# Optimization experiments

Measured on AMD Instinct MI355X. Metric: run time of the kernel, lower is better.

Reference implementation:

```python
import jax, jax.numpy as jnp
import numpy as np

MASK_FILL = -987654321.0


def rotate_every_two(x):
    # pairs (x0, x1) -> (-x1, x0), interleaved back along last dim
    x1 = x[..., 0::2]
    x2 = x[..., 1::2]
    return jnp.stack((-x2, x1), axis=-1).reshape(x.shape)


def setup_inputs() -> dict:
    key = jax.random.key(0)
    ks = jax.random.split(key, 6)
    b, n, dim = 64, 197, 768
    heads, dim_head = 12, 64
    inner = heads * dim_head
    x = jax.random.normal(ks[0], (b, n, dim), dtype=jnp.float32)
    pos_emb = jax.random.normal(ks[1], (1, n, dim_head), dtype=jnp.float32)
    w_qkv = jax.random.normal(ks[2], (dim, 3 * inner), dtype=jnp.float32) * (dim ** -0.5)
    scale = jnp.full((heads,), dim_head ** -0.5, dtype=jnp.float32)
    w_out = jax.random.normal(ks[3], (inner, dim), dtype=jnp.float32) * (inner ** -0.5)
    b_out = jnp.zeros((dim,), dtype=jnp.float32)
    return {"x": x, "pos_emb": pos_emb, "w_qkv": w_qkv, "scale": scale,
            "w_out": w_out, "b_out": b_out}


def reference(x, pos_emb, w_qkv, scale, w_out, b_out):
    b, n, dim = x.shape
    h = scale.shape[0]
    qkv = x @ w_qkv                         # [b, n, 3*inner]
    q, k, v = jnp.split(qkv, 3, axis=-1)
    dh = q.shape[-1] // h
    to_heads = lambda t: t.reshape(b, n, h, dh).transpose(0, 2, 1, 3)  # bhnd
    q, k, v = to_heads(q), to_heads(k), to_heads(v)

    # RoPE: pos_emb [1, n, (2 * dh/2)] -> sin/cos [n, dh/2] -> interleave to [n, dh]
    sc = pos_emb[0].reshape(n, 2, dh // 2)
    sin = jnp.repeat(sc[:, 0], 2, axis=-1)  # [n, dh]
    cos = jnp.repeat(sc[:, 1], 2, axis=-1)
    q = q * cos + rotate_every_two(q) * sin
    k = k * cos + rotate_every_two(k) * sin

    # per-head learnable scale
    dots = jnp.einsum('bhid,bhjd->bhij', q, k) * scale[None, :, None, None]
    # diagonal (LSA) mask
    eye = jnp.eye(n, dtype=bool)
    dots = jnp.where(eye, MASK_FILL, dots)

    attn = jax.nn.softmax(dots, axis=-1)
    out = jnp.einsum('bhij,bhjd->bhid', attn, v)
    out = out.transpose(0, 2, 1, 3).reshape(b, n, h * dh)
    return out @ w_out + b_out
```

## Files before the change

kernel.cpp:

```cpp
#include <hip/hip_runtime.h>
#include <math.h>

#define MASK_FILL_F (-987654321.0f)

typedef unsigned short u16;
typedef unsigned int   u32;

constexpr int Bb   = 64;
constexpr int Ntok = 197;
constexpr int Dim  = 768;
constexpr int Heads= 12;
constexpr int Dh   = 64;
constexpr int Nq3  = 2304;
constexpr int Rows = 12608;
constexpr int Mpad = 12672;

using f32x4  = __attribute__((ext_vector_type(4))) float;
using bf16x8 = __attribute__((ext_vector_type(8))) short;

__device__ __forceinline__ u16 f2bf(float f) {
  u32 u = __float_as_uint(f);
  u = (u + 0x7fffu + ((u >> 16) & 1u)) >> 16;
  return (u16)u;
}

__device__ __forceinline__ void stage16(const void* gp, void* lp) {
  __builtin_amdgcn_global_load_lds(
      (const __attribute__((address_space(1))) u32*)gp,
      (__attribute__((address_space(3))) u32*)lp, 16, 0, 0);
}

__device__ __forceinline__ int sigma6(int M) {
  return (M & 0x23) | (((M >> 3) & 1) << 4) | (((M >> 2) & 1) << 3) |
         (((M >> 4) & 1) << 2);
}

__global__ __launch_bounds__(256) void cvt_bf16(const float* __restrict__ in,
                                                u16* __restrict__ out, int n4) {
  const int i = blockIdx.x * 256 + threadIdx.x;
  if (i < n4) {
    const float4 v = *(const float4*)&in[(size_t)i * 4];
    ushort4 u;
    u.x = f2bf(v.x); u.y = f2bf(v.y); u.z = f2bf(v.z); u.w = f2bf(v.w);
    *(ushort4*)&out[(size_t)i * 4] = u;
  }
}

__global__ __launch_bounds__(256) void transpose_cvt(const float* __restrict__ in,
                                                     u16* __restrict__ out,
                                                     int R, int C) {
  __shared__ float t[32][33];
  const int c0 = blockIdx.x * 32, r0 = blockIdx.y * 32;
  const int tx = threadIdx.x & 31, ty = threadIdx.x >> 5;
#pragma unroll
  for (int rr = ty; rr < 32; rr += 8)
    t[rr][tx] = in[(size_t)(r0 + rr) * C + c0 + tx];
  __syncthreads();
#pragma unroll
  for (int cc = ty; cc < 32; cc += 8)
    out[(size_t)(c0 + cc) * R + r0 + tx] = f2bf(t[tx][cc]);
}

__global__ __launch_bounds__(256) void vtrans(const u16* __restrict__ qkvB,
                                              u16* __restrict__ vT) {
  __shared__ u16 t[64 * 72];
  const int jt = blockIdx.x, bh = blockIdx.y;
  const int b = bh / Heads, h = bh % Heads;
  const int j0 = jt * 64;
  const int tid = threadIdx.x;

  for (int idx = tid; idx < 512; idx += 256) {
    const int jr = idx >> 3, c8 = (idx & 7) * 8;
    const int j = j0 + jr;
    uint4 u = make_uint4(0u, 0u, 0u, 0u);
    if (j < Ntok)
      u = *(const uint4*)(qkvB + (size_t)(b * Ntok + j) * Nq3 + 2 * Dim + h * Dh + c8);
    *(uint4*)&t[jr * 72 + c8] = u;
  }
  __syncthreads();
  for (int idx = tid; idx < 512; idx += 256) {
    const int d = idx >> 3, j8 = (idx & 7) * 8;
    ushort4 lo, hi;
    lo.x = t[(j8 + 0) * 72 + d]; lo.y = t[(j8 + 1) * 72 + d];
    lo.z = t[(j8 + 2) * 72 + d]; lo.w = t[(j8 + 3) * 72 + d];
    hi.x = t[(j8 + 4) * 72 + d]; hi.y = t[(j8 + 5) * 72 + d];
    hi.z = t[(j8 + 6) * 72 + d]; hi.w = t[(j8 + 7) * 72 + d];
    u16* dst = vT + ((size_t)bh * 64 + d) * 256 + j0 + j8;
    *(ushort4*)dst       = lo;
    *(ushort4*)(dst + 4) = hi;
  }
}

constexpr int Kc  = 768;
constexpr int NKT = Kc / 64;
#define KTC(x) ((x) < NKT ? (x) : (NKT - 1))

#define BARM() asm volatile("s_barrier" ::: "memory")
#define VMW4() asm volatile("s_waitcnt vmcnt(4)" ::: "memory")

#define STGA(chunk, kt, BUF) \
  stage16(Ag + (size_t)(m0 + (chunk) * 8 + srow) * Kc + (kt) * 64 + scol, \
          &As[BUF][(chunk) * 512])
#define STGB(chunk, kt, BUF) \
  stage16(Bg + (size_t)(n0 + (chunk) * 8 + srow) * Kc + (kt) * 64 + scol, \
          &Bs[BUF][(chunk) * 512])

#define RDA(BUF, MH) \
  _Pragma("unroll") for (int m_ = 0; m_ < 4; ++m_) \
  _Pragma("unroll") for (int k_ = 0; k_ < 2; ++k_) \
    af[m_][k_] = *(const bf16x8*)&As[BUF][(wr * 128 + (MH) * 64 + m_ * 16 + tx) * 64 \
                                          + (((k_ * 4 + qd) ^ sx) * 8)];
#define RDB(BUF, NH, BFR) \
  _Pragma("unroll") for (int n_ = 0; n_ < 2; ++n_) \
  _Pragma("unroll") for (int k_ = 0; k_ < 2; ++k_) \
    BFR[n_][k_] = *(const bf16x8*)&Bs[BUF][(wc * 64 + (NH) * 32 + n_ * 16 + tx) * 64 \
                                           + (((k_ * 4 + qd) ^ sx) * 8)];

#define MM(MH, NH, BFR) \
  __builtin_amdgcn_s_setprio(1); \
  _Pragma("unroll") for (int m_ = 0; m_ < 4; ++m_) \
  _Pragma("unroll") for (int n_ = 0; n_ < 2; ++n_) \
  _Pragma("unroll") for (int k_ = 0; k_ < 2; ++k_) \
    acc[(MH) * 4 + m_][(NH) * 2 + n_] = __builtin_amdgcn_mfma_f32_16x16x32_bf16( \
        af[m_][k_], BFR[n_][k_], acc[(MH) * 4 + m_][(NH) * 2 + n_], 0, 0, 0); \
  __builtin_amdgcn_s_setprio(0);

template<int TN>
__global__ __launch_bounds__(512, 2) void gemm8p(
    const u16* __restrict__ Ag, const u16* __restrict__ Bg,
    u16* __restrict__ Cb, int Nn, int nwg,
    const float* __restrict__ pe)
{
  __shared__ u16 As[2][256 * 64];
  __shared__ u16 Bs[2][256 * 64];

  const int tid = threadIdx.x, lane = tid & 63, w = tid >> 6;

  const int orig = blockIdx.x;
  const int q8 = nwg >> 3, r8 = nwg & 7;
  const int xcd = orig & 7, sub = orig >> 3;
  const int wgid = (xcd < r8 ? xcd * (q8 + 1) : r8 * (q8 + 1) + (xcd - r8) * q8) + sub;
  const int tm = wgid / TN, tn = wgid % TN;
  const int m0 = tm * 256, n0 = tn * 256;

  const int wr = w >> 2, wc = w & 3;
  const int tx = lane & 15, qd = lane >> 4, sx = tx & 7;

  const int srow = lane >> 3;
  const int scol = ((lane & 7) ^ srow) * 8;
  const int b0 = (w >> 1) * 8 + (w & 1) * 2;

  STGA(w, 0, 0);        STGA(16 + w, 0, 0);
  STGB(b0 + 4, 0, 0);   STGB(b0 + 5, 0, 0);
  STGA(8 + w, 0, 0);    STGA(24 + w, 0, 0);
  STGB(b0, 0, 0);       STGB(b0 + 1, 0, 0);
  STGA(w, 1, 1);        STGA(16 + w, 1, 1);
  STGB(b0 + 4, 1, 1);   STGB(b0 + 5, 1, 1);
  VMW4();
  BARM();

  f32x4  acc[8][4] = {};
  bf16x8 af[4][2], bf0[2][2], bf1[2][2];

#pragma unroll 1
  for (int i = 0; i < NKT / 2; ++i) {
    const int u = 2 * i;
    RDA(0, 0); RDB(0, 0, bf0);
    STGA(8 + w, u + 1, 1); STGA(24 + w, u + 1, 1);
    BARM(); MM(0, 0, bf0); BARM();
    RDB(0, 1, bf1);
    STGB(b0, u + 1, 1); STGB(b0 + 1, u + 1, 1);
    BARM(); MM(0, 1, bf1); BARM();
    RDA(0, 1);
    STGA(w, KTC(u + 2), 0); STGA(16 + w, KTC(u + 2), 0);
    BARM(); MM(1, 1, bf1); BARM();
    STGB(b0 + 4, KTC(u + 2), 0); STGB(b0 + 5, KTC(u + 2), 0);
    BARM(); MM(1, 0, bf0); VMW4(); BARM();
    RDA(1, 0); RDB(1, 0, bf0);
    STGA(8 + w, KTC(u + 2), 0); STGA(24 + w, KTC(u + 2), 0);
    BARM(); MM(0, 0, bf0); BARM();
    RDB(1, 1, bf1);
    STGB(b0, KTC(u + 2), 0); STGB(b0 + 1, KTC(u + 2), 0);
    BARM(); MM(0, 1, bf1); BARM();
    RDA(1, 1);
    STGA(w, KTC(u + 3), 1); STGA(16 + w, KTC(u + 3), 1);
    BARM(); MM(1, 1, bf1); BARM();
    STGB(b0 + 4, KTC(u + 3), 1); STGB(b0 + 5, KTC(u + 3), 1);
    BARM(); MM(1, 0, bf0); VMW4(); BARM();
  }

  const bool dorot = (n0 < 2 * Dim);
#pragma unroll
  for (int mi = 0; mi < 8; ++mi) {
    const int rbase = m0 + wr * 128 + mi * 16 + qd * 4;
    int iq[4];
#pragma unroll
    for (int r = 0; r < 4; ++r) iq[r] = (rbase + r) % Ntok;
#pragma unroll
    for (int ni = 0; ni < 4; ++ni) {
      const int col = n0 + wc * 64 + ni * 16 + tx;
      const int mm  = (col & 63) >> 1;
      const int odd = col & 1;
#pragma unroll
      for (int r = 0; r < 4; ++r) {
        float v = acc[mi][ni][r];
        float res = v;
        if (dorot) {
          const float other = __shfl_xor(v, 1, 64);
          const float sn = pe[iq[r] * 64 + mm];
          const float c2 = pe[iq[r] * 64 + 32 + mm];
          res = odd ? (v * c2 + other * sn) : (v * c2 - other * sn);
        }
        Cb[(size_t)(rbase + r) * Nn + col] = f2bf(res);
      }
    }
  }
}

__global__ __launch_bounds__(256) void gemm_bt1(
    const u16* __restrict__ Ag, const u16* __restrict__ Bg,
    float* __restrict__ C, int K, int Nn, const float* __restrict__ bias)
{
  __shared__ u16 As[128 * 32];
  __shared__ u16 Bs[128 * 32];
  const int tid = threadIdx.x, lane = tid & 63, w = tid >> 6;
  const int m0 = blockIdx.y * 128, n0 = blockIdx.x * 128;
  const int wm = (w & 1) * 64, wn = (w >> 1) * 64;
  const int tx = lane & 15, qk = lane >> 4;
  const int rs = lane >> 2, cs = (lane & 3) * 8;

  f32x4 acc[4][4] = {};

  for (int k0 = 0; k0 < K; k0 += 32) {
#pragma unroll
    for (int t = 0; t < 2; ++t) {
      const int r0 = w * 16 + t * 64;
      stage16(Ag + (size_t)(m0 + r0 + rs) * K + k0 + cs, &As[r0 * 32]);
      stage16(Bg + (size_t)(n0 + r0 + rs) * K + k0 + cs, &Bs[r0 * 32]);
    }
    __syncthreads();
    bf16x8 af[4], bf[4];
#pragma unroll
    for (int f = 0; f < 4; ++f) {
      af[f] = *(const bf16x8*)&As[(wm + f * 16 + tx) * 32 + qk * 8];
      bf[f] = *(const bf16x8*)&Bs[(wn + f * 16 + tx) * 32 + qk * 8];
    }
#pragma unroll
    for (int fm = 0; fm < 4; ++fm)
#pragma unroll
      for (int fn = 0; fn < 4; ++fn)
        acc[fm][fn] = __builtin_amdgcn_mfma_f32_16x16x32_bf16(
            af[fm], bf[fn], acc[fm][fn], 0, 0, 0);
    __syncthreads();
  }

#pragma unroll
  for (int fm = 0; fm < 4; ++fm) {
    const int rbase = m0 + wm + fm * 16 + qk * 4;
#pragma unroll
    for (int fn = 0; fn < 4; ++fn) {
      const int col = n0 + wn + fn * 16 + tx;
      const float bv = bias[col];
#pragma unroll
      for (int r = 0; r < 4; ++r) {
        const int row = rbase + r;
        if (row < Rows) C[(size_t)row * Nn + col] = acc[fm][fn][r] + bv;
      }
    }
  }
}

constexpr int LS = 72;

__global__ __launch_bounds__(512) void attn8(
    const u16* __restrict__ qkvB, const u16* __restrict__ vT,
    const float* __restrict__ scale, u16* __restrict__ outB)
{
  __shared__ u16 ks [64 * LS];
  __shared__ u16 vts[64 * LS];

  const int bh = blockIdx.x;
  const int b = bh / Heads, h = bh % Heads;
  const float sc = scale[h];
  const int tid = threadIdx.x, lane = tid & 63, w = tid >> 6;
  const int tx = lane & 15, q = lane >> 4;
  const size_t rowbase = (size_t)b * Ntok;

  const int Ms = tid >> 3, c8s = (tid & 7) * 8;
  const u16* kgp = qkvB + (rowbase + sigma6(Ms)) * (size_t)Nq3 + Dim + h * Dh + c8s;
  const u16* vgp = vT + ((size_t)bh * 64 + Ms) * 256 + c8s;

  bf16x8 bq[2][2];
#pragma unroll
  for (int g = 0; g < 2; ++g)
#pragma unroll
    for (int kk = 0; kk < 2; ++kk)
      bq[g][kk] = *(const bf16x8*)(qkvB +
          (rowbase + 32 * w + 16 * g + tx) * (size_t)Nq3 + h * Dh + kk * 32 + q * 8);

  uint4 kreg = *(const uint4*)kgp;
  uint4 vreg = *(const uint4*)vgp;

  float l_part[2] = {0.f, 0.f};
  f32x4 oacc[2][4] = {};

  for (int jt = 0; jt < 4; ++jt) {
    const int j0 = jt * 64;
    __syncthreads();
    *(uint4*)&ks [Ms * LS + c8s] = kreg;
    *(uint4*)&vts[Ms * LS + c8s] = vreg;
    __syncthreads();
    if (jt < 3) {
      kreg = *(const uint4*)(kgp + (size_t)(jt + 1) * 64 * Nq3);
      vreg = *(const uint4*)(vgp + (jt + 1) * 64);
    }

#pragma unroll
    for (int g = 0; g < 2; ++g) {
      f32x4 sT[4] = {};
#pragma unroll
      for (int kk = 0; kk < 2; ++kk)
#pragma unroll
        for (int jb = 0; jb < 4; ++jb) {
          const bf16x8 ka = *(const bf16x8*)&ks[(jb * 16 + tx) * LS + kk * 32 + q * 8];
          sT[jb] = __builtin_amdgcn_mfma_f32_16x16x32_bf16(ka, bq[g][kk], sT[jb], 0, 0, 0);
        }

      const int ig = 32 * w + 16 * g + tx;
      union { bf16x8 v; u16 e[8]; } pk[2];
      float lp = 0.f;
#pragma unroll
      for (int jb = 0; jb < 4; ++jb)
#pragma unroll
        for (int r = 0; r < 4; ++r) {
          const int jg = j0 + 32 * (jb >> 1) + 8 * q + 4 * (jb & 1) + r;
          const float s = fminf(sT[jb][r] * sc, 80.f);
          const bool bad = (jg >= Ntok) || (jg == ig);
          const float p = bad ? 0.f : __expf(s);
          lp += p;
          pk[jb >> 1].e[(jb & 1) * 4 + r] = f2bf(p);
        }
      l_part[g] += lp;

#pragma unroll
      for (int kk = 0; kk < 2; ++kk)
#pragma unroll
        for (int nb = 0; nb < 4; ++nb) {
          const bf16x8 vb = *(const bf16x8*)&vts[(nb * 16 + tx) * LS + kk * 32 + q * 8];
          oacc[g][nb] = __builtin_amdgcn_mfma_f32_16x16x32_bf16(pk[kk].v, vb,
                                                               oacc[g][nb], 0, 0, 0);
        }
    }
  }

#pragma unroll
  for (int g = 0; g < 2; ++g) {
    float l = l_part[g];
    l += __shfl_xor(l, 16, 64);
    l += __shfl_xor(l, 32, 64);
    const float linv = 1.0f / l;
#pragma unroll
    for (int r = 0; r < 4; ++r) {
      const float lr = __shfl(linv, 4 * q + r, 64);
      const int igr = 32 * w + 16 * g + 4 * q + r;
      if (igr < Ntok) {
#pragma unroll
        for (int nb = 0; nb < 4; ++nb)
          outB[(rowbase + igr) * (size_t)Dim + h * Dh + nb * 16 + tx] =
              f2bf(oacc[g][nb][r] * lr);
      }
    }
  }
}

extern "C" void kernel_launch(void* const* d_in, const int* in_sizes, int n_in,
                              void* d_out, int out_size, void* d_ws, size_t ws_size,
                              hipStream_t stream) {
  const float* x     = (const float*)d_in[0];
  const float* pe    = (const float*)d_in[1];
  const float* w_qkv = (const float*)d_in[2];
  const float* scale = (const float*)d_in[3];
  const float* w_out = (const float*)d_in[4];
  const float* b_out = (const float*)d_in[5];
  float* out = (float*)d_out;

  u16* xb    = (u16*)d_ws;
  u16* wqkvT = xb    + (size_t)Mpad * Dim;
  u16* woutT = wqkvT + (size_t)Nq3 * Dim;
  u16* qkvB  = woutT + (size_t)Dim * Dim;
  u16* attnB = qkvB  + (size_t)Mpad * Nq3;
  u16* vT    = attnB + (size_t)Mpad * Dim;

  cvt_bf16<<<(Rows * Dim / 4 + 255) / 256, 256, 0, stream>>>(x, xb, Rows * Dim / 4);
  transpose_cvt<<<dim3(Nq3 / 32, Dim / 32), 256, 0, stream>>>(w_qkv, wqkvT, Dim, Nq3);
  transpose_cvt<<<dim3(Dim / 32, Dim / 32), 256, 0, stream>>>(w_out, woutT, Dim, Dim);

  constexpr int NWG0 = 50 * 9;
  gemm8p<9><<<NWG0, 512, 0, stream>>>(xb, wqkvT, qkvB, Nq3, NWG0, pe);

  vtrans<<<dim3(4, Bb * Heads), 256, 0, stream>>>(qkvB, vT);

  attn8<<<Bb * Heads, 512, 0, stream>>>(qkvB, vT, scale, attnB);

  gemm_bt1<<<dim3(Dim / 128, Mpad / 128), 256, 0, stream>>>(
      attnB, woutT, out, Dim, Dim, b_out);
}
```

Before: 273.4 us.

## Split attention query rows across 16 waves and 1024-thread blocks

The attention kernel now runs 1024 threads per block, so each wave owns one 16-row query group instead of two, with 13 active waves covering the 197 tokens. The K and V tile staging is split so half the threads load K and half load V, which removes one of the two global loads per thread. s_setprio is raised around the MFMA sections. This trades fewer registers per thread and more waves for latency hiding against 3 idle compute waves and more threads taking part in each barrier.

```diff
diff --git a/kernel.cpp b/kernel.cpp
--- a/kernel.cpp
+++ b/kernel.cpp
@@ -272,7 +272,7 @@
 
 constexpr int LS = 72;
 
-__global__ __launch_bounds__(512) void attn8(
+__global__ __launch_bounds__(1024) void attn16(
     const u16* __restrict__ qkvB, const u16* __restrict__ vT,
     const float* __restrict__ scale, u16* __restrict__ outB)
 {
@@ -285,48 +285,49 @@
   const int tid = threadIdx.x, lane = tid & 63, w = tid >> 6;
   const int tx = lane & 15, q = lane >> 4;
   const size_t rowbase = (size_t)b * Ntok;
-
-  const int Ms = tid >> 3, c8s = (tid & 7) * 8;
-  const u16* kgp = qkvB + (rowbase + sigma6(Ms)) * (size_t)Nq3 + Dim + h * Dh + c8s;
-  const u16* vgp = vT + ((size_t)bh * 64 + Ms) * 256 + c8s;
-
-  bf16x8 bq[2][2];
-#pragma unroll
-  for (int g = 0; g < 2; ++g)
+  const bool active = (w < 13);
+
+  const int Ms = (tid & 511) >> 3, c8s = (tid & 7) * 8;
+  const bool isK = tid < 512;
+  const u16* sgp = isK
+      ? qkvB + (rowbase + sigma6(Ms)) * (size_t)Nq3 + Dim + h * Dh + c8s
+      : vT + ((size_t)bh * 64 + Ms) * 256 + c8s;
+  const size_t sstep = isK ? (size_t)64 * Nq3 : (size_t)64;
+  u16* slds = (isK ? ks : vts) + Ms * LS + c8s;
+
+  bf16x8 bq[2];
+  if (active) {
 #pragma unroll
     for (int kk = 0; kk < 2; ++kk)
-      bq[g][kk] = *(const bf16x8*)(qkvB +
-          (rowbase + 32 * w + 16 * g + tx) * (size_t)Nq3 + h * Dh + kk * 32 + q * 8);
-
-  uint4 kreg = *(const uint4*)kgp;
-  uint4 vreg = *(const uint4*)vgp;
-
-  float l_part[2] = {0.f, 0.f};
-  f32x4 oacc[2][4] = {};
+      bq[kk] = *(const bf16x8*)(qkvB +
+          (rowbase + 16 * w + tx) * (size_t)Nq3 + h * Dh + kk * 32 + q * 8);
+  }
+
+  uint4 sreg = *(const uint4*)sgp;
+
+  float l_part = 0.f;
+  f32x4 oacc[4] = {};
 
   for (int jt = 0; jt < 4; ++jt) {
     const int j0 = jt * 64;
     __syncthreads();
-    *(uint4*)&ks [Ms * LS + c8s] = kreg;
-    *(uint4*)&vts[Ms * LS + c8s] = vreg;
+    *(uint4*)slds = sreg;
     __syncthreads();
-    if (jt < 3) {
-      kreg = *(const uint4*)(kgp + (size_t)(jt + 1) * 64 * Nq3);
-      vreg = *(const uint4*)(vgp + (jt + 1) * 64);
-    }
-
-#pragma unroll
-    for (int g = 0; g < 2; ++g) {
+    if (jt < 3) sreg = *(const uint4*)(sgp + (size_t)(jt + 1) * sstep);
+
+    if (active) {
       f32x4 sT[4] = {};
+      __builtin_amdgcn_s_setprio(1);
 #pragma unroll
       for (int kk = 0; kk < 2; ++kk)
 #pragma unroll
         for (int jb = 0; jb < 4; ++jb) {
           const bf16x8 ka = *(const bf16x8*)&ks[(jb * 16 + tx) * LS + kk * 32 + q * 8];
-          sT[jb] = __builtin_amdgcn_mfma_f32_16x16x32_bf16(ka, bq[g][kk], sT[jb], 0, 0, 0);
+          sT[jb] = __builtin_amdgcn_mfma_f32_16x16x32_bf16(ka, bq[kk], sT[jb], 0, 0, 0);
         }
-
-      const int ig = 32 * w + 16 * g + tx;
+      __builtin_amdgcn_s_setprio(0);
+
+      const int ig = 16 * w + tx;
       union { bf16x8 v; u16 e[8]; } pk[2];
       float lp = 0.f;
 #pragma unroll
@@ -340,34 +341,35 @@
           lp += p;
           pk[jb >> 1].e[(jb & 1) * 4 + r] = f2bf(p);
         }
-      l_part[g] += lp;
-
+      l_part += lp;
+
+      __builtin_amdgcn_s_setprio(1);
 #pragma unroll
       for (int kk = 0; kk < 2; ++kk)
 #pragma unroll
         for (int nb = 0; nb < 4; ++nb) {
           const bf16x8 vb = *(const bf16x8*)&vts[(nb * 16 + tx) * LS + kk * 32 + q * 8];
-          oacc[g][nb] = __builtin_amdgcn_mfma_f32_16x16x32_bf16(pk[kk].v, vb,
-                                                               oacc[g][nb], 0, 0, 0);
+          oacc[nb] = __builtin_amdgcn_mfma_f32_16x16x32_bf16(pk[kk].v, vb,
+                                                            oacc[nb], 0, 0, 0);
         }
-    }
-  }
-
-#pragma unroll
-  for (int g = 0; g < 2; ++g) {
-    float l = l_part[g];
+      __builtin_amdgcn_s_setprio(0);
+    }
+  }
+
+  if (active) {
+    float l = l_part;
     l += __shfl_xor(l, 16, 64);
     l += __shfl_xor(l, 32, 64);
     const float linv = 1.0f / l;
 #pragma unroll
     for (int r = 0; r < 4; ++r) {
       const float lr = __shfl(linv, 4 * q + r, 64);
-      const int igr = 32 * w + 16 * g + 4 * q + r;
+      const int igr = 16 * w + 4 * q + r;
       if (igr < Ntok) {
 #pragma unroll
         for (int nb = 0; nb < 4; ++nb)
           outB[(rowbase + igr) * (size_t)Dim + h * Dh + nb * 16 + tx] =
-              f2bf(oacc[g][nb][r] * lr);
+              f2bf(oacc[nb][r] * lr);
       }
     }
   }
@@ -400,7 +402,7 @@
 
   vtrans<<<dim3(4, Bb * Heads), 256, 0, stream>>>(qkvB, vT);
 
-  attn8<<<Bb * Heads, 512, 0, stream>>>(qkvB, vT, scale, attnB);
+  attn16<<<Bb * Heads, 1024, 0, stream>>>(qkvB, vT, scale, attnB);
 
   gemm_bt1<<<dim3(Dim / 128, Mpad / 128), 256, 0, stream>>>(
       attnB, woutT, out, Dim, Dim, b_out);
```

Measured after the change: 273.3 us. Within noise of the previous version (-0.0%).
